# Kernel optimization log

Hardware: AMD Instinct MI355X
Metric: run time of the kernel (lower is better)

## Reference

```python
import jax, jax.numpy as jnp
import numpy as np

K = 128      # classes
CIN = 128    # ch_in
CL = 128     # ch_latent
B, H, W = 8, 1, 8192
SLOPE = 0.01 # F.leaky_relu default
EPS = 1e-5   # BatchNorm eps


def lrelu(x):
    return jnp.where(x >= 0, x, SLOPE * x)


def conv1x1(x, w, b):
    # x: (B,C,H,W), w: (O,C), b: (O,)
    return jnp.einsum('bchw,oc->bohw', x, w) + b[None, :, None, None]


def bn_eval(x, gamma, beta, mean, var):
    scale = gamma * jax.lax.rsqrt(var + EPS)
    return x * scale[None, :, None, None] + (beta - mean * scale)[None, :, None, None]


def setup_inputs() -> dict:
    key = jax.random.key(0)
    ks = jax.random.split(key, 16)
    def w(k, shape, fan_in):
        return jax.random.normal(k, shape, jnp.float32) / np.sqrt(fan_in)
    return {
        'x_in': jax.random.normal(ks[0], (B, CIN, H, W), jnp.float32),
        'cl1_w': w(ks[1], (CL, CIN), CIN), 'cl1_b': jnp.zeros((CL,), jnp.float32),
        'bn1_gamma': jnp.ones((CL,), jnp.float32), 'bn1_beta': jnp.zeros((CL,), jnp.float32),
        'bn1_mean': 0.1 * jax.random.normal(ks[2], (CL,), jnp.float32),
        'bn1_var': jax.random.uniform(ks[3], (CL,), jnp.float32, 0.5, 1.5),
        'cl2_w': w(ks[4], (CL, CL), CL), 'cl2_b': jnp.zeros((CL,), jnp.float32),
        'cl3_w': w(ks[5], (K + 1, CL), CL), 'cl3_b': jnp.zeros((K + 1,), jnp.float32),
        'reg1_w': w(ks[6], (CL, CIN), CIN), 'reg1_b': jnp.zeros((CL,), jnp.float32),
        'bnr_gamma': jnp.ones((CL,), jnp.float32), 'bnr_beta': jnp.zeros((CL,), jnp.float32),
        'bnr_mean': 0.1 * jax.random.normal(ks[7], (CL,), jnp.float32),
        'bnr_var': jax.random.uniform(ks[8], (CL,), jnp.float32, 0.5, 1.5),
        'cm2_w': w(ks[9], (K, CL, 32), CL), 'cm2_b': jnp.zeros((K, 32), jnp.float32),
        'cm3_w': w(ks[10], (K, 32, 1), 32), 'cm3_b': jnp.zeros((K, 1), jnp.float32),
    }


def reference(x_in, cl1_w, cl1_b, bn1_gamma, bn1_beta, bn1_mean, bn1_var,
              cl2_w, cl2_b, cl3_w, cl3_b,
              reg1_w, reg1_b, bnr_gamma, bnr_beta, bnr_mean, bnr_var,
              cm2_w, cm2_b, cm3_w, cm3_b):
    # classification branch
    x = lrelu(bn_eval(conv1x1(x_in, cl1_w, cl1_b), bn1_gamma, bn1_beta, bn1_mean, bn1_var))
    x = lrelu(conv1x1(x, cl2_w, cl2_b))
    x = conv1x1(x, cl3_w, cl3_b)                    # (B, K+1, H, W)
    logits = x[:, :K]
    mask = lrelu(x[:, -1:])                          # (B,1,H,W)
    inds = jnp.argmax(logits, axis=1)                # (B,H,W) int
    inds_r = inds.reshape(-1).astype(jnp.int32)      # (N,)
    xr = lrelu(bn_eval(conv1x1(x_in, reg1_w, reg1_b), bnr_gamma, bnr_beta, bnr_mean, bnr_var))
    # torch: transpose(1,3).reshape(-1, C)  -> (B,W,H,C) flatten
    xr = jnp.transpose(xr, (0, 3, 2, 1)).reshape(-1, CL)   # (N, CL)
    # CondMul 1: per-pixel gathered weight (N,CL,32)
    h = lrelu(jnp.einsum('ni,nio->no', xr, cm2_w[inds_r]) + cm2_b[inds_r])
    # CondMul 2: (N,32)->(N,1)
    reg = jnp.einsum('ni,nio->no', h, cm3_w[inds_r]) + cm3_b[inds_r]
    reg = reg.reshape(B, 1, 1, -1)                   # (B,1,1,H*W)
    x_real = (inds[:, None].astype(jnp.float32) + reg) * (1.0 / K)
    return x_real, mask
```

## Files before the change

kernel.cpp:

```cpp
#include <hip/hip_runtime.h>
#include <math.h>

#define NPOS 65536
#define NCH  128
#define DELTA 0.008f
#define HPAD 16

#define OFF_XR   0u
#define OFF_W1T  8388608u
#define OFF_W2T  (OFF_W1T + 16384u)
#define OFF_W3T  (OFF_W2T + 16384u)
#define OFF_B1F  (OFF_W3T + 16384u)
#define OFF_BRF  (OFF_B1F + 128u)
#define OFF_B2F  (OFF_BRF + 128u)
#define OFF_B3F  (OFF_B2F + 128u)
#define OFF_BF16 (OFF_B3F + 132u)
#define OFF_INT  (OFF_BF16 + 329728u)

#define UW1H 0u
#define UW1L 16384u
#define UWRH 32768u
#define UWRL 49152u
#define UW2H 65536u
#define UW2L 81920u
#define UW3H 98304u
#define UW3L 116736u
#define UW2K 135168u

#define NST 2080

typedef short bf16x8 __attribute__((ext_vector_type(8)));
typedef float f32x4 __attribute__((ext_vector_type(4)));
#define MFMA16 __builtin_amdgcn_mfma_f32_16x16x32_bf16

__device__ __forceinline__ float lrelu(float v) { return v >= 0.0f ? v : 0.01f * v; }
__device__ __forceinline__ unsigned short f2bf(float f) {
    unsigned u = __float_as_uint(f);
    return (unsigned short)((u + 0x7fffu + ((u >> 16) & 1u)) >> 16);
}
__device__ __forceinline__ float bf2f(unsigned short h) {
    return __uint_as_float(((unsigned)h) << 16);
}
__device__ __forceinline__ unsigned long long pack4(unsigned short a, unsigned short b,
                                                    unsigned short c, unsigned short d) {
    return (unsigned long long)a | ((unsigned long long)b << 16)
         | ((unsigned long long)c << 32) | ((unsigned long long)d << 48);
}

__global__ void k_prep(const float* __restrict__ cl1_w, const float* __restrict__ cl1_b,
                       const float* __restrict__ g1, const float* __restrict__ be1,
                       const float* __restrict__ mu1, const float* __restrict__ va1,
                       const float* __restrict__ cl2_w, const float* __restrict__ cl2_b,
                       const float* __restrict__ cl3_w, const float* __restrict__ cl3_b,
                       const float* __restrict__ reg1_w, const float* __restrict__ reg1_b,
                       const float* __restrict__ gr, const float* __restrict__ ber,
                       const float* __restrict__ mur, const float* __restrict__ var_,
                       const float* __restrict__ cm2w,
                       float* __restrict__ ws_f, unsigned short* __restrict__ wbf,
                       int* __restrict__ hist, int* __restrict__ fixcnt)
{
    const int bid = blockIdx.x;
    const int t = threadIdx.x;
    if (bid >= 128) {
        __shared__ float tl[32 * 132];
        int k = bid - 128;
        #pragma unroll
        for (int i = 0; i < 32; ++i) {
            float v = cm2w[(unsigned)k * 4096u + i * 128 + t];
            int ci = i * 4 + (t >> 5), o = t & 31;
            tl[o * 132 + ci] = v;
        }
        __syncthreads();
        #pragma unroll
        for (int i = 0; i < 32; ++i)
            wbf[UW2K + (unsigned)k * 4096u + i * 128 + t] = f2bf(tl[i * 132 + t]);
        return;
    }
    int tid = bid * 128 + t;
    int cin = tid >> 7, cout = tid & 127;
    float s1 = g1[cout] / sqrtf(va1[cout] + 1e-5f);
    float sr = gr[cout] / sqrtf(var_[cout] + 1e-5f);
    float w1 = cl1_w[cout * 128 + cin] * s1;
    float wr = reg1_w[cout * 128 + cin] * sr;
    float w2 = cl2_w[cout * 128 + cin];
    float w3 = cl3_w[cout * 128 + cin];
    ws_f[OFF_W1T + tid] = w1;
    ws_f[OFF_W2T + tid] = w2;
    ws_f[OFF_W3T + tid] = w3;
    int j = cout * 128 + cin;
    unsigned short h;
    h = f2bf(w1); wbf[UW1H + j] = h; wbf[UW1L + j] = f2bf(w1 - bf2f(h));
    h = f2bf(wr); wbf[UWRH + j] = h; wbf[UWRL + j] = f2bf(wr - bf2f(h));
    h = f2bf(w2); wbf[UW2H + j] = h; wbf[UW2L + j] = f2bf(w2 - bf2f(h));
    h = f2bf(w3); wbf[UW3H + j] = h; wbf[UW3L + j] = f2bf(w3 - bf2f(h));
    if (tid < 2048) {
        int r = tid >> 7, ci = tid & 127;
        float v = (r == 0) ? cl3_w[128 * 128 + ci] : 0.0f;
        int jj = (128 + r) * 128 + ci;
        h = f2bf(v); wbf[UW3H + jj] = h; wbf[UW3L + jj] = f2bf(v - bf2f(h));
    }
    if (tid < 128) {
        float s1b = g1[tid] / sqrtf(va1[tid] + 1e-5f);
        float srb = gr[tid] / sqrtf(var_[tid] + 1e-5f);
        ws_f[OFF_B1F + tid] = cl1_b[tid] * s1b + be1[tid] - mu1[tid] * s1b;
        ws_f[OFF_BRF + tid] = reg1_b[tid] * srb + ber[tid] - mur[tid] * srb;
        ws_f[OFF_B2F + tid] = cl2_b[tid];
        hist[tid * HPAD] = 0;
    }
    if (tid < 129) ws_f[OFF_B3F + tid] = cl3_b[tid];
    if (tid == 0) fixcnt[0] = 0;
}

__global__ __launch_bounds__(256, 4)
void k_fused(const float* __restrict__ X, const float* __restrict__ wsf,
             const unsigned short* __restrict__ wbf,
             unsigned short* __restrict__ XRB, float* __restrict__ out_mask,
             int* __restrict__ inds, int* __restrict__ fixcnt,
             int* __restrict__ fixlist)
{
    __shared__ __align__(16) unsigned short XBh[64 * 136];
    __shared__ __align__(16) unsigned short XBl[64 * 136];
    __shared__ float sm1[4 * 64];
    __shared__ float sm2[4 * 64];
    __shared__ int   si1[4 * 64];

    const int t = threadIdx.x;
    const int lane = t & 63;
    const int cl16 = lane & 15;
    const int q8 = (lane >> 4) * 8;
    const int q4 = (lane >> 4) * 4;
    const int wv = __builtin_amdgcn_readfirstlane(t >> 6);
    const unsigned nt64 = blockIdx.x * 64u;
    const unsigned base = nt64 + (nt64 >> 13) * 1040384u;

    const unsigned short* W1H = wbf + UW1H; const unsigned short* W1L = wbf + UW1L;
    const unsigned short* WRH = wbf + UWRH; const unsigned short* WRL = wbf + UWRL;
    const unsigned short* W2H = wbf + UW2H; const unsigned short* W2L = wbf + UW2L;
    const unsigned short* W3H = wbf + UW3H; const unsigned short* W3L = wbf + UW3L;
    const float* b1f = wsf + OFF_B1F;
    const float* brf = wsf + OFF_BRF;
    const float* b2f = wsf + OFF_B2F;
    const float* b3f = wsf + OFF_B3F;

    const f32x4 vzero = {0.f, 0.f, 0.f, 0.f};

    {
        const int pos = t & 63, cig = t >> 6;
        #pragma unroll
        for (int l = 0; l < 8; ++l) {
            int ci0 = cig * 32 + l * 4;
            float v0 = X[base + (unsigned)(ci0 + 0) * 8192u + pos];
            float v1 = X[base + (unsigned)(ci0 + 1) * 8192u + pos];
            float v2 = X[base + (unsigned)(ci0 + 2) * 8192u + pos];
            float v3 = X[base + (unsigned)(ci0 + 3) * 8192u + pos];
            unsigned short h0 = f2bf(v0), h1 = f2bf(v1), h2 = f2bf(v2), h3 = f2bf(v3);
            unsigned long long ph = pack4(h0, h1, h2, h3);
            unsigned long long pl = pack4(f2bf(v0 - bf2f(h0)), f2bf(v1 - bf2f(h1)),
                                          f2bf(v2 - bf2f(h2)), f2bf(v3 - bf2f(h3)));
            *(unsigned long long*)&XBh[pos * 136 + ci0] = ph;
            *(unsigned long long*)&XBl[pos * 136 + ci0] = pl;
        }
    }
    __syncthreads();

    f32x4 acc[2][4];

    #pragma unroll
    for (int m = 0; m < 2; ++m)
        #pragma unroll
        for (int n = 0; n < 4; ++n) acc[m][n] = vzero;
    #pragma unroll
    for (int kt = 0; kt < 4; ++kt) {
        bf16x8 Bh[4], Bl[4];
        #pragma unroll
        for (int n = 0; n < 4; ++n) {
            int bo = (n * 16 + cl16) * 136 + kt * 32 + q8;
            Bh[n] = *(const bf16x8*)&XBh[bo];
            Bl[n] = *(const bf16x8*)&XBl[bo];
        }
        #pragma unroll
        for (int m = 0; m < 2; ++m) {
            int ao = (wv * 32 + m * 16 + cl16) * 128 + kt * 32 + q8;
            bf16x8 arh = *(const bf16x8*)&WRH[ao], arl = *(const bf16x8*)&WRL[ao];
            #pragma unroll
            for (int n = 0; n < 4; ++n) {
                acc[m][n] = MFMA16(arh, Bl[n], acc[m][n], 0, 0, 0);
                acc[m][n] = MFMA16(arl, Bh[n], acc[m][n], 0, 0, 0);
                acc[m][n] = MFMA16(arh, Bh[n], acc[m][n], 0, 0, 0);
            }
        }
    }
    {
        #pragma unroll
        for (int m = 0; m < 2; ++m) {
            int cb = wv * 32 + m * 16 + q4;
            float br0 = brf[cb], br1 = brf[cb + 1], br2 = brf[cb + 2], br3 = brf[cb + 3];
            #pragma unroll
            for (int n = 0; n < 4; ++n) {
                unsigned pb = (nt64 + n * 16 + cl16) * 128u + cb;
                ushort4 xo;
                xo.x = f2bf(lrelu(acc[m][n][0] + br0));
                xo.y = f2bf(lrelu(acc[m][n][1] + br1));
                xo.z = f2bf(lrelu(acc[m][n][2] + br2));
                xo.w = f2bf(lrelu(acc[m][n][3] + br3));
                *(ushort4*)&XRB[pb] = xo;
            }
        }
    }

    #pragma unroll
    for (int m = 0; m < 2; ++m)
        #pragma unroll
        for (int n = 0; n < 4; ++n) acc[m][n] = vzero;
    #pragma unroll
    for (int kt = 0; kt < 4; ++kt) {
        bf16x8 Bh[4], Bl[4];
        #pragma unroll
        for (int n = 0; n < 4; ++n) {
            int bo = (n * 16 + cl16) * 136 + kt * 32 + q8;
            Bh[n] = *(const bf16x8*)&XBh[bo];
            Bl[n] = *(const bf16x8*)&XBl[bo];
        }
        #pragma unroll
        for (int m = 0; m < 2; ++m) {
            int ao = (wv * 32 + m * 16 + cl16) * 128 + kt * 32 + q8;
            bf16x8 a1h = *(const bf16x8*)&W1H[ao], a1l = *(const bf16x8*)&W1L[ao];
            #pragma unroll
            for (int n = 0; n < 4; ++n) {
                acc[m][n] = MFMA16(a1h, Bl[n], acc[m][n], 0, 0, 0);
                acc[m][n] = MFMA16(a1l, Bh[n], acc[m][n], 0, 0, 0);
                acc[m][n] = MFMA16(a1h, Bh[n], acc[m][n], 0, 0, 0);
            }
        }
    }
    __syncthreads();
    {
        #pragma unroll
        for (int m = 0; m < 2; ++m) {
            int cb = wv * 32 + m * 16 + q4;
            float b0 = b1f[cb], b1 = b1f[cb + 1], b2 = b1f[cb + 2], b3 = b1f[cb + 3];
            #pragma unroll
            for (int n = 0; n < 4; ++n) {
                float v0 = lrelu(acc[m][n][0] + b0), v1 = lrelu(acc[m][n][1] + b1);
                float v2 = lrelu(acc[m][n][2] + b2), v3 = lrelu(acc[m][n][3] + b3);
                unsigned short h0 = f2bf(v0), h1 = f2bf(v1), h2 = f2bf(v2), h3 = f2bf(v3);
                unsigned long long ph = pack4(h0, h1, h2, h3);
                unsigned long long pl = pack4(f2bf(v0 - bf2f(h0)), f2bf(v1 - bf2f(h1)),
                                              f2bf(v2 - bf2f(h2)), f2bf(v3 - bf2f(h3)));
                int idx = (n * 16 + cl16) * 136 + cb;
                *(unsigned long long*)&XBh[idx] = ph;
                *(unsigned long long*)&XBl[idx] = pl;
            }
        }
    }
    __syncthreads();

    #pragma unroll
    for (int m = 0; m < 2; ++m)
        #pragma unroll
        for (int n = 0; n < 4; ++n) acc[m][n] = vzero;
    #pragma unroll
    for (int kt = 0; kt < 4; ++kt) {
        bf16x8 Bh[4], Bl[4];
        #pragma unroll
        for (int n = 0; n < 4; ++n) {
            int bo = (n * 16 + cl16) * 136 + kt * 32 + q8;
            Bh[n] = *(const bf16x8*)&XBh[bo];
            Bl[n] = *(const bf16x8*)&XBl[bo];
        }
        #pragma unroll
        for (int m = 0; m < 2; ++m) {
            int ao = (wv * 32 + m * 16 + cl16) * 128 + kt * 32 + q8;
            bf16x8 ah = *(const bf16x8*)&W2H[ao], al = *(const bf16x8*)&W2L[ao];
            #pragma unroll
            for (int n = 0; n < 4; ++n) {
                acc[m][n] = MFMA16(ah, Bl[n], acc[m][n], 0, 0, 0);
                acc[m][n] = MFMA16(al, Bh[n], acc[m][n], 0, 0, 0);
                acc[m][n] = MFMA16(ah, Bh[n], acc[m][n], 0, 0, 0);
            }
        }
    }
    __syncthreads();
    {
        #pragma unroll
        for (int m = 0; m < 2; ++m) {
            int cb = wv * 32 + m * 16 + q4;
            float b0 = b2f[cb], b1 = b2f[cb + 1], b2 = b2f[cb + 2], b3 = b2f[cb + 3];
            #pragma unroll
            for (int n = 0; n < 4; ++n) {
                float v0 = lrelu(acc[m][n][0] + b0), v1 = lrelu(acc[m][n][1] + b1);
                float v2 = lrelu(acc[m][n][2] + b2), v3 = lrelu(acc[m][n][3] + b3);
                unsigned short h0 = f2bf(v0), h1 = f2bf(v1), h2 = f2bf(v2), h3 = f2bf(v3);
                unsigned long long ph = pack4(h0, h1, h2, h3);
                unsigned long long pl = pack4(f2bf(v0 - bf2f(h0)), f2bf(v1 - bf2f(h1)),
                                              f2bf(v2 - bf2f(h2)), f2bf(v3 - bf2f(h3)));
                int idx = (n * 16 + cl16) * 136 + cb;
                *(unsigned long long*)&XBh[idx] = ph;
                *(unsigned long long*)&XBl[idx] = pl;
            }
        }
    }
    __syncthreads();

    f32x4 accM = vzero;
    #pragma unroll
    for (int m = 0; m < 2; ++m)
        #pragma unroll
        for (int n = 0; n < 4; ++n) acc[m][n] = vzero;
    #pragma unroll
    for (int kt = 0; kt < 4; ++kt) {
        bf16x8 Bh[4], Bl[4];
        #pragma unroll
        for (int n = 0; n < 4; ++n) {
            int bo = (n * 16 + cl16) * 136 + kt * 32 + q8;
            Bh[n] = *(const bf16x8*)&XBh[bo];
            Bl[n] = *(const bf16x8*)&XBl[bo];
        }
        #pragma unroll
        for (int m = 0; m < 2; ++m) {
            int ao = (wv * 32 + m * 16 + cl16) * 128 + kt * 32 + q8;
            bf16x8 ah = *(const bf16x8*)&W3H[ao], al = *(const bf16x8*)&W3L[ao];
            #pragma unroll
            for (int n = 0; n < 4; ++n) {
                acc[m][n] = MFMA16(ah, Bl[n], acc[m][n], 0, 0, 0);
                acc[m][n] = MFMA16(al, Bh[n], acc[m][n], 0, 0, 0);
                acc[m][n] = MFMA16(ah, Bh[n], acc[m][n], 0, 0, 0);
            }
        }
        {
            int boM = (wv * 16 + cl16) * 136 + kt * 32 + q8;
            bf16x8 BhM = *(const bf16x8*)&XBh[boM];
            bf16x8 BlM = *(const bf16x8*)&XBl[boM];
            int ao = (128 + cl16) * 128 + kt * 32 + q8;
            bf16x8 ah = *(const bf16x8*)&W3H[ao], al = *(const bf16x8*)&W3L[ao];
            accM = MFMA16(ah, BlM, accM, 0, 0, 0);
            accM = MFMA16(al, BhM, accM, 0, 0, 0);
            accM = MFMA16(ah, BhM, accM, 0, 0, 0);
        }
    }

    {
        float bb[2][4];
        #pragma unroll
        for (int m = 0; m < 2; ++m) {
            int cb = wv * 32 + m * 16 + q4;
            bb[m][0] = b3f[cb]; bb[m][1] = b3f[cb + 1];
            bb[m][2] = b3f[cb + 2]; bb[m][3] = b3f[cb + 3];
        }
        float m1[4], m2[4]; int i1[4];
        #pragma unroll
        for (int n = 0; n < 4; ++n) {
            m1[n] = -1e30f; m2[n] = -1e30f; i1[n] = 0;
            #pragma unroll
            for (int m = 0; m < 2; ++m) {
                int cb = wv * 32 + m * 16 + q4;
                #pragma unroll
                for (int r = 0; r < 4; ++r) {
                    float v = acc[m][n][r] + bb[m][r];
                    if (v > m1[n]) { m2[n] = m1[n]; m1[n] = v; i1[n] = cb + r; }
                    else if (v > m2[n]) m2[n] = v;
                }
            }
        }
        #pragma unroll
        for (int off = 16; off <= 32; off <<= 1) {
            #pragma unroll
            for (int n = 0; n < 4; ++n) {
                float om1 = __shfl_xor(m1[n], off);
                float om2 = __shfl_xor(m2[n], off);
                int   oi1 = __shfl_xor(i1[n], off);
                if (om1 > m1[n] || (om1 == m1[n] && oi1 < i1[n])) {
                    m2[n] = fmaxf(m1[n], om2); m1[n] = om1; i1[n] = oi1;
                } else {
                    m2[n] = fmaxf(m2[n], om1);
                }
            }
        }
        if ((lane >> 4) == 0) {
            #pragma unroll
            for (int n = 0; n < 4; ++n) {
                sm1[wv * 64 + n * 16 + cl16] = m1[n];
                sm2[wv * 64 + n * 16 + cl16] = m2[n];
                si1[wv * 64 + n * 16 + cl16] = i1[n];
            }
        }
    }
    if ((lane >> 4) == 0) {
        float mb = b3f[128];
        out_mask[nt64 + wv * 16 + cl16] = lrelu(accM[0] + mb);
    }
    __syncthreads();
    if (t < 64) {
        float m1 = sm1[t], m2 = sm2[t];
        int i1 = si1[t];
        #pragma unroll
        for (int w = 1; w < 4; ++w) {
            float v1 = sm1[w * 64 + t];
            float v2 = sm2[w * 64 + t];
            int   vi = si1[w * 64 + t];
            if (v1 > m1) { m2 = fmaxf(m1, v2); m1 = v1; i1 = vi; }
            else         { m2 = fmaxf(m2, v1); }
        }
        int n = nt64 + t;
        inds[n] = i1;
        if (m1 - m2 < DELTA) {
            int slot = atomicAdd(fixcnt, 1);
            fixlist[slot] = n;
        }
    }
}

__global__ __launch_bounds__(256, 4)
void k_fix(const float* __restrict__ X, const float* __restrict__ wsf,
           const int* __restrict__ fixcnt, const int* __restrict__ fixlist,
           int* __restrict__ inds)
{
    const int cnt = fixcnt[0];
    const int t = threadIdx.x;
    const int lane = t & 63;
    const int wv = t >> 6;
    const float* W1T = wsf + OFF_W1T;
    const float* W2T = wsf + OFF_W2T;
    const float* W3T = wsf + OFF_W3T;
    const float* b1f = wsf + OFF_B1F;
    const float* b2f = wsf + OFF_B2F;
    const float* b3f = wsf + OFF_B3F;

    for (int idx = blockIdx.x * 4 + wv; idx < cnt; idx += 1024) {
        int n = fixlist[idx];
        const float* xb = X + (unsigned)(n >> 13) * 1048576u + (unsigned)(n & 8191);
        float x0 = xb[(unsigned)lane * 8192u];
        float x1 = xb[(unsigned)(64 + lane) * 8192u];
        float a0, a1;
        a0 = 0.f; a1 = 0.f;
        for (int ci = 0; ci < 64; ++ci) {
            float xv = __shfl(x0, ci);
            const float* wr = W1T + ci * 128;
            a0 = fmaf(wr[lane], xv, a0);
            a1 = fmaf(wr[64 + lane], xv, a1);
        }
        for (int ci = 0; ci < 64; ++ci) {
            float xv = __shfl(x1, ci);
            const float* wr = W1T + (64 + ci) * 128;
            a0 = fmaf(wr[lane], xv, a0);
            a1 = fmaf(wr[64 + lane], xv, a1);
        }
        x0 = lrelu(a0 + b1f[lane]); x1 = lrelu(a1 + b1f[64 + lane]);
        a0 = 0.f; a1 = 0.f;
        for (int ci = 0; ci < 64; ++ci) {
            float xv = __shfl(x0, ci);
            const float* wr = W2T + ci * 128;
            a0 = fmaf(wr[lane], xv, a0);
            a1 = fmaf(wr[64 + lane], xv, a1);
        }
        for (int ci = 0; ci < 64; ++ci) {
            float xv = __shfl(x1, ci);
            const float* wr = W2T + (64 + ci) * 128;
            a0 = fmaf(wr[lane], xv, a0);
            a1 = fmaf(wr[64 + lane], xv, a1);
        }
        x0 = lrelu(a0 + b2f[lane]); x1 = lrelu(a1 + b2f[64 + lane]);
        a0 = 0.f; a1 = 0.f;
        for (int ci = 0; ci < 64; ++ci) {
            float xv = __shfl(x0, ci);
            const float* wr = W3T + ci * 128;
            a0 = fmaf(wr[lane], xv, a0);
            a1 = fmaf(wr[64 + lane], xv, a1);
        }
        for (int ci = 0; ci < 64; ++ci) {
            float xv = __shfl(x1, ci);
            const float* wr = W3T + (64 + ci) * 128;
            a0 = fmaf(wr[lane], xv, a0);
            a1 = fmaf(wr[64 + lane], xv, a1);
        }
        float L0 = a0 + b3f[lane], L1 = a1 + b3f[64 + lane];
        float v; int id;
        if (L0 >= L1) { v = L0; id = lane; } else { v = L1; id = 64 + lane; }
        #pragma unroll
        for (int off = 1; off < 64; off <<= 1) {
            float ov = __shfl_xor(v, off);
            int   oi = __shfl_xor(id, off);
            if (ov > v || (ov == v && oi < id)) { v = ov; id = oi; }
        }
        if (lane == 0) inds[n] = id;
    }
}

__global__ void k_hist(const int* __restrict__ inds, int* __restrict__ hist)
{
    __shared__ int lh[128];
    int t = threadIdx.x;
    if (t < 128) lh[t] = 0;
    __syncthreads();
    atomicAdd(&lh[inds[blockIdx.x * 256 + t]], 1);
    __syncthreads();
    if (t < 128 && lh[t] > 0) atomicAdd(&hist[t * HPAD], lh[t]);
}

__global__ void k_scan(const int* __restrict__ hist, int* __restrict__ off,
                       int* __restrict__ cur, int* __restrict__ tiles,
                       int* __restrict__ ntt)
{
    __shared__ int s[128];
    __shared__ int s2[128];
    int t = threadIdx.x;
    int v = hist[t * HPAD];
    int ntk = (v + 63) >> 6;
    s[t] = v;
    s2[t] = ntk;
    __syncthreads();
    for (int d = 1; d < 128; d <<= 1) {
        int a  = (t >= d) ? s[t - d]  : 0;
        int a2 = (t >= d) ? s2[t - d] : 0;
        __syncthreads();
        s[t] += a;
        s2[t] += a2;
        __syncthreads();
    }
    off[t] = s[t] - v;
    cur[t * HPAD] = s[t] - v;
    int tb = s2[t] - ntk;
    for (int j = 0; j < ntk; ++j)
        tiles[tb + j] = (t << 16) | j;
    if (t == 127) ntt[0] = s2[127];
}

__global__ void k_scatter(const int* __restrict__ inds, int* __restrict__ cur,
                          int* __restrict__ bucket)
{
    __shared__ int lh[128];
    __shared__ int gb[128];
    int t = threadIdx.x;
    if (t < 128) lh[t] = 0;
    __syncthreads();
    int n = blockIdx.x * 256 + t;
    int id = inds[n];
    int r = atomicAdd(&lh[id], 1);
    __syncthreads();
    if (t < 128 && lh[t] > 0) gb[t] = atomicAdd(&cur[t * HPAD], lh[t]);
    __syncthreads();
    bucket[gb[id] + r] = n;
}

__global__ __launch_bounds__(256, 4)
void k_reg(const unsigned short* __restrict__ XRB, const unsigned short* __restrict__ wbf,
           const float* __restrict__ cm2b, const float* __restrict__ cm3w,
           const float* __restrict__ cm3b, const int* __restrict__ hist,
           const int* __restrict__ off, const int* __restrict__ bucket,
           const int* __restrict__ tiles, const int* __restrict__ ntt,
           float* __restrict__ out)
{
    __shared__ __align__(16) unsigned short XP[4 * NST];
    __shared__ float red[64];
    int bid = blockIdx.x;
    if (bid >= ntt[0]) return;
    int desc = tiles[bid];
    int k = desc >> 16;
    int start = (desc & 0xffff) << 6;
    int cnt = hist[k * HPAD];
    int base = off[k];
    int t = threadIdx.x;
    int lane = t & 63;
    int wv = __builtin_amdgcn_readfirstlane(t >> 6);
    const int n16 = lane & 15;
    const int quad = lane >> 4;

    {
        int rs = t >> 2;
        int q = t & 3;
        int sidx = start + rs;
        if (sidx >= cnt) sidx = cnt - 1;
        int n = bucket[base + sidx];
        const uint4* src = (const uint4*)(XRB + (unsigned)n * 128u + q * 32);
        uint4 a0 = src[0], a1 = src[1], a2 = src[2], a3 = src[3];
        unsigned db = (rs >> 4) * NST + q * 512 + (rs & 15) * 8;
        *(uint4*)&XP[db]       = a0;
        *(uint4*)&XP[db + 128] = a1;
        *(uint4*)&XP[db + 256] = a2;
        *(uint4*)&XP[db + 384] = a3;
    }
    __syncthreads();

    const unsigned short* wb = wbf + UW2K + (unsigned)k * 4096u;
    bf16x8 Bf[2][4];
    #pragma unroll
    for (int nf = 0; nf < 2; ++nf)
        #pragma unroll
        for (int kt = 0; kt < 4; ++kt)
            Bf[nf][kt] = *(const bf16x8*)&wb[(nf * 16 + n16) * 128 + kt * 32 + quad * 8];

    const f32x4 vzero = {0.f, 0.f, 0.f, 0.f};
    f32x4 acc[2];
    acc[0] = vzero; acc[1] = vzero;
    #pragma unroll
    for (int kt = 0; kt < 4; ++kt) {
        bf16x8 Af = *(const bf16x8*)&XP[wv * NST + kt * 512 + lane * 8];
        #pragma unroll
        for (int nf = 0; nf < 2; ++nf)
            acc[nf] = MFMA16(Af, Bf[nf][kt], acc[nf], 0, 0, 0);
    }

    float b2a = cm2b[k * 32 + n16], b2b = cm2b[k * 32 + 16 + n16];
    float w3a = cm3w[k * 32 + n16], w3b = cm3w[k * 32 + 16 + n16];
    #pragma unroll
    for (int r = 0; r < 4; ++r) {
        float p = lrelu(acc[0][r] + b2a) * w3a
                + lrelu(acc[1][r] + b2b) * w3b;
        p += __shfl_xor(p, 1);
        p += __shfl_xor(p, 2);
        p += __shfl_xor(p, 4);
        p += __shfl_xor(p, 8);
        if (n16 == 0)
            red[wv * 16 + quad * 4 + r] = p;
    }
    __syncthreads();
    if (t < 64 && start + t < cnt) {
        int n2 = bucket[base + start + t];
        out[n2] = ((float)k + red[t] + cm3b[k]) * (1.0f / 128.0f);
    }
}

extern "C" void kernel_launch(void* const* d_in, const int* in_sizes, int n_in,
                              void* d_out, int out_size, void* d_ws, size_t ws_size,
                              hipStream_t stream)
{
    (void)in_sizes; (void)n_in; (void)out_size; (void)ws_size;
    const float* x_in   = (const float*)d_in[0];
    const float* cl1_w  = (const float*)d_in[1];
    const float* cl1_b  = (const float*)d_in[2];
    const float* g1     = (const float*)d_in[3];
    const float* be1    = (const float*)d_in[4];
    const float* mu1    = (const float*)d_in[5];
    const float* va1    = (const float*)d_in[6];
    const float* cl2_w  = (const float*)d_in[7];
    const float* cl2_b  = (const float*)d_in[8];
    const float* cl3_w  = (const float*)d_in[9];
    const float* cl3_b  = (const float*)d_in[10];
    const float* reg1_w = (const float*)d_in[11];
    const float* reg1_b = (const float*)d_in[12];
    const float* gr     = (const float*)d_in[13];
    const float* ber    = (const float*)d_in[14];
    const float* mur    = (const float*)d_in[15];
    const float* var_   = (const float*)d_in[16];
    const float* cm2w   = (const float*)d_in[17];
    const float* cm2b   = (const float*)d_in[18];
    const float* cm3w   = (const float*)d_in[19];
    const float* cm3b   = (const float*)d_in[20];

    float* ws_f = (float*)d_ws;
    unsigned short* XRB = (unsigned short*)(ws_f + OFF_XR);
    unsigned short* wbf = (unsigned short*)(ws_f + OFF_BF16);
    int*   wsi    = (int*)(ws_f + OFF_INT);
    int*   inds   = wsi;
    int*   hist   = inds + 65536;
    int*   offb   = hist + 2048;
    int*   cur    = offb + 128;
    int*   ntt    = cur + 2048;
    int*   fixcnt = ntt + 4;
    int*   tiles  = fixcnt + 4;
    int*   fixlist= tiles + 1536;
    int*   bucket = fixlist + 65536;
    float* out = (float*)d_out;

    hipLaunchKernelGGL(k_prep, dim3(256), dim3(128), 0, stream,
                       cl1_w, cl1_b, g1, be1, mu1, va1, cl2_w, cl2_b, cl3_w, cl3_b,
                       reg1_w, reg1_b, gr, ber, mur, var_, cm2w, ws_f, wbf, hist, fixcnt);
    hipLaunchKernelGGL(k_fused, dim3(1024), dim3(256), 0, stream,
                       x_in, ws_f, wbf, XRB, out + 65536, inds, fixcnt, fixlist);
    hipLaunchKernelGGL(k_fix, dim3(256), dim3(256), 0, stream,
                       x_in, ws_f, fixcnt, fixlist, inds);
    hipLaunchKernelGGL(k_hist, dim3(256), dim3(256), 0, stream, inds, hist);
    hipLaunchKernelGGL(k_scan, dim3(1), dim3(128), 0, stream,
                       hist, offb, cur, tiles, ntt);
    hipLaunchKernelGGL(k_scatter, dim3(256), dim3(256), 0, stream, inds, cur, bucket);
    hipLaunchKernelGGL(k_reg, dim3(1536), dim3(256), 0, stream,
                       XRB, wbf, cm2b, cm3w, cm3b, hist, offb, bucket, tiles, ntt, out);
}
```

Before: 221.3 us.

## Fold fix, histogram and scan kernels into fused, scatter and regression kernels

The separate k_fix, k_hist and k_scan launches are removed. Near-tie argmax recomputation and the per-class histogram now run at the tail of k_fused, using a block-local fix list. The prefix scan over class counts is recomputed redundantly in every k_scatter and k_reg block instead of in a single-block kernel, and k_prep writes the transposed fp32 weights with coalesced reads. This cuts seven launches to four and their serialization gaps, in exchange for redundant scans and uneven tail work inside k_fused blocks.

Result: faster. 205.3 us (-7.2%).

```diff
diff --git a/kernel.cpp b/kernel.cpp
--- a/kernel.cpp
+++ b/kernel.cpp
@@ -57,7 +57,7 @@
                        const float* __restrict__ mur, const float* __restrict__ var_,
                        const float* __restrict__ cm2w,
                        float* __restrict__ ws_f, unsigned short* __restrict__ wbf,
-                       int* __restrict__ hist, int* __restrict__ fixcnt)
+                       int* __restrict__ hist, int* __restrict__ cur)
 {
     const int bid = blockIdx.x;
     const int t = threadIdx.x;
@@ -76,53 +76,56 @@
             wbf[UW2K + (unsigned)k * 4096u + i * 128 + t] = f2bf(tl[i * 132 + t]);
         return;
     }
-    int tid = bid * 128 + t;
-    int cin = tid >> 7, cout = tid & 127;
+    const int cout = bid;
+    const int cin = t;
+    const int row = cout * 128 + cin;
     float s1 = g1[cout] / sqrtf(va1[cout] + 1e-5f);
     float sr = gr[cout] / sqrtf(var_[cout] + 1e-5f);
-    float w1 = cl1_w[cout * 128 + cin] * s1;
-    float wr = reg1_w[cout * 128 + cin] * sr;
-    float w2 = cl2_w[cout * 128 + cin];
-    float w3 = cl3_w[cout * 128 + cin];
-    ws_f[OFF_W1T + tid] = w1;
-    ws_f[OFF_W2T + tid] = w2;
-    ws_f[OFF_W3T + tid] = w3;
-    int j = cout * 128 + cin;
+    float w1 = cl1_w[row] * s1;
+    float wr = reg1_w[row] * sr;
+    float w2 = cl2_w[row];
+    float w3 = cl3_w[row];
+    ws_f[OFF_W1T + cin * 128 + cout] = w1;
+    ws_f[OFF_W2T + cin * 128 + cout] = w2;
+    ws_f[OFF_W3T + cin * 128 + cout] = w3;
     unsigned short h;
-    h = f2bf(w1); wbf[UW1H + j] = h; wbf[UW1L + j] = f2bf(w1 - bf2f(h));
-    h = f2bf(wr); wbf[UWRH + j] = h; wbf[UWRL + j] = f2bf(wr - bf2f(h));
-    h = f2bf(w2); wbf[UW2H + j] = h; wbf[UW2L + j] = f2bf(w2 - bf2f(h));
-    h = f2bf(w3); wbf[UW3H + j] = h; wbf[UW3L + j] = f2bf(w3 - bf2f(h));
-    if (tid < 2048) {
-        int r = tid >> 7, ci = tid & 127;
-        float v = (r == 0) ? cl3_w[128 * 128 + ci] : 0.0f;
-        int jj = (128 + r) * 128 + ci;
+    h = f2bf(w1); wbf[UW1H + row] = h; wbf[UW1L + row] = f2bf(w1 - bf2f(h));
+    h = f2bf(wr); wbf[UWRH + row] = h; wbf[UWRL + row] = f2bf(wr - bf2f(h));
+    h = f2bf(w2); wbf[UW2H + row] = h; wbf[UW2L + row] = f2bf(w2 - bf2f(h));
+    h = f2bf(w3); wbf[UW3H + row] = h; wbf[UW3L + row] = f2bf(w3 - bf2f(h));
+    if (bid < 16) {
+        float v = (bid == 0) ? cl3_w[128 * 128 + t] : 0.0f;
+        int jj = (128 + bid) * 128 + t;
         h = f2bf(v); wbf[UW3H + jj] = h; wbf[UW3L + jj] = f2bf(v - bf2f(h));
     }
-    if (tid < 128) {
-        float s1b = g1[tid] / sqrtf(va1[tid] + 1e-5f);
-        float srb = gr[tid] / sqrtf(var_[tid] + 1e-5f);
-        ws_f[OFF_B1F + tid] = cl1_b[tid] * s1b + be1[tid] - mu1[tid] * s1b;
-        ws_f[OFF_BRF + tid] = reg1_b[tid] * srb + ber[tid] - mur[tid] * srb;
-        ws_f[OFF_B2F + tid] = cl2_b[tid];
-        hist[tid * HPAD] = 0;
-    }
-    if (tid < 129) ws_f[OFF_B3F + tid] = cl3_b[tid];
-    if (tid == 0) fixcnt[0] = 0;
+    if (bid == 0) {
+        float s1b = g1[t] / sqrtf(va1[t] + 1e-5f);
+        float srb = gr[t] / sqrtf(var_[t] + 1e-5f);
+        ws_f[OFF_B1F + t] = cl1_b[t] * s1b + be1[t] - mu1[t] * s1b;
+        ws_f[OFF_BRF + t] = reg1_b[t] * srb + ber[t] - mur[t] * srb;
+        ws_f[OFF_B2F + t] = cl2_b[t];
+        ws_f[OFF_B3F + t] = cl3_b[t];
+        hist[t * HPAD] = 0;
+        cur[t * HPAD] = 0;
+    }
+    if (bid == 1 && t == 0) ws_f[OFF_B3F + 128] = cl3_b[128];
 }
 
 __global__ __launch_bounds__(256, 4)
 void k_fused(const float* __restrict__ X, const float* __restrict__ wsf,
              const unsigned short* __restrict__ wbf,
              unsigned short* __restrict__ XRB, float* __restrict__ out_mask,
-             int* __restrict__ inds, int* __restrict__ fixcnt,
-             int* __restrict__ fixlist)
+             int* __restrict__ inds, int* __restrict__ hist)
 {
     __shared__ __align__(16) unsigned short XBh[64 * 136];
     __shared__ __align__(16) unsigned short XBl[64 * 136];
     __shared__ float sm1[4 * 64];
     __shared__ float sm2[4 * 64];
     __shared__ int   si1[4 * 64];
+    __shared__ int   locid[64];
+    __shared__ int   flist[64];
+    __shared__ int   fcntS;
+    __shared__ int   lh[128];
 
     const int t = threadIdx.x;
     const int lane = t & 63;
@@ -143,6 +146,8 @@
     const float* b3f = wsf + OFF_B3F;
 
     const f32x4 vzero = {0.f, 0.f, 0.f, 0.f};
+
+    if (t == 0) fcntS = 0;
 
     {
         const int pos = t & 63, cig = t >> 6;
@@ -403,141 +408,110 @@
         }
         int n = nt64 + t;
         inds[n] = i1;
+        locid[t] = i1;
         if (m1 - m2 < DELTA) {
-            int slot = atomicAdd(fixcnt, 1);
-            fixlist[slot] = n;
-        }
-    }
-}
-
-__global__ __launch_bounds__(256, 4)
-void k_fix(const float* __restrict__ X, const float* __restrict__ wsf,
-           const int* __restrict__ fixcnt, const int* __restrict__ fixlist,
-           int* __restrict__ inds)
-{
-    const int cnt = fixcnt[0];
-    const int t = threadIdx.x;
-    const int lane = t & 63;
-    const int wv = t >> 6;
-    const float* W1T = wsf + OFF_W1T;
-    const float* W2T = wsf + OFF_W2T;
-    const float* W3T = wsf + OFF_W3T;
-    const float* b1f = wsf + OFF_B1F;
-    const float* b2f = wsf + OFF_B2F;
-    const float* b3f = wsf + OFF_B3F;
-
-    for (int idx = blockIdx.x * 4 + wv; idx < cnt; idx += 1024) {
-        int n = fixlist[idx];
-        const float* xb = X + (unsigned)(n >> 13) * 1048576u + (unsigned)(n & 8191);
-        float x0 = xb[(unsigned)lane * 8192u];
-        float x1 = xb[(unsigned)(64 + lane) * 8192u];
-        float a0, a1;
-        a0 = 0.f; a1 = 0.f;
-        for (int ci = 0; ci < 64; ++ci) {
-            float xv = __shfl(x0, ci);
-            const float* wr = W1T + ci * 128;
-            a0 = fmaf(wr[lane], xv, a0);
-            a1 = fmaf(wr[64 + lane], xv, a1);
-        }
-        for (int ci = 0; ci < 64; ++ci) {
-            float xv = __shfl(x1, ci);
-            const float* wr = W1T + (64 + ci) * 128;
-            a0 = fmaf(wr[lane], xv, a0);
-            a1 = fmaf(wr[64 + lane], xv, a1);
-        }
-        x0 = lrelu(a0 + b1f[lane]); x1 = lrelu(a1 + b1f[64 + lane]);
-        a0 = 0.f; a1 = 0.f;
-        for (int ci = 0; ci < 64; ++ci) {
-            float xv = __shfl(x0, ci);
-            const float* wr = W2T + ci * 128;
-            a0 = fmaf(wr[lane], xv, a0);
-            a1 = fmaf(wr[64 + lane], xv, a1);
-        }
-        for (int ci = 0; ci < 64; ++ci) {
-            float xv = __shfl(x1, ci);
-            const float* wr = W2T + (64 + ci) * 128;
-            a0 = fmaf(wr[lane], xv, a0);
-            a1 = fmaf(wr[64 + lane], xv, a1);
-        }
-        x0 = lrelu(a0 + b2f[lane]); x1 = lrelu(a1 + b2f[64 + lane]);
-        a0 = 0.f; a1 = 0.f;
-        for (int ci = 0; ci < 64; ++ci) {
-            float xv = __shfl(x0, ci);
-            const float* wr = W3T + ci * 128;
-            a0 = fmaf(wr[lane], xv, a0);
-            a1 = fmaf(wr[64 + lane], xv, a1);
-        }
-        for (int ci = 0; ci < 64; ++ci) {
-            float xv = __shfl(x1, ci);
-            const float* wr = W3T + (64 + ci) * 128;
-            a0 = fmaf(wr[lane], xv, a0);
-            a1 = fmaf(wr[64 + lane], xv, a1);
-        }
-        float L0 = a0 + b3f[lane], L1 = a1 + b3f[64 + lane];
-        float v; int id;
-        if (L0 >= L1) { v = L0; id = lane; } else { v = L1; id = 64 + lane; }
-        #pragma unroll
-        for (int off = 1; off < 64; off <<= 1) {
-            float ov = __shfl_xor(v, off);
-            int   oi = __shfl_xor(id, off);
-            if (ov > v || (ov == v && oi < id)) { v = ov; id = oi; }
-        }
-        if (lane == 0) inds[n] = id;
-    }
-}
-
-__global__ void k_hist(const int* __restrict__ inds, int* __restrict__ hist)
-{
-    __shared__ int lh[128];
-    int t = threadIdx.x;
+            int slot = atomicAdd(&fcntS, 1);
+            flist[slot] = t;
+        }
+    }
+    __syncthreads();
+
+    {
+        const int fc = fcntS;
+        const float* W1T = wsf + OFF_W1T;
+        const float* W2T = wsf + OFF_W2T;
+        const float* W3T = wsf + OFF_W3T;
+        for (int i = wv; i < fc; i += 4) {
+            int pos = flist[i];
+            int n = nt64 + pos;
+            const float* xb = X + (unsigned)(n >> 13) * 1048576u + (unsigned)(n & 8191);
+            float x0 = xb[(unsigned)lane * 8192u];
+            float x1 = xb[(unsigned)(64 + lane) * 8192u];
+            float a0, a1;
+            a0 = 0.f; a1 = 0.f;
+            for (int ci = 0; ci < 64; ++ci) {
+                float xv = __shfl(x0, ci);
+                const float* wr = W1T + ci * 128;
+                a0 = fmaf(wr[lane], xv, a0);
+                a1 = fmaf(wr[64 + lane], xv, a1);
+            }
+            for (int ci = 0; ci < 64; ++ci) {
+                float xv = __shfl(x1, ci);
+                const float* wr = W1T + (64 + ci) * 128;
+                a0 = fmaf(wr[lane], xv, a0);
+                a1 = fmaf(wr[64 + lane], xv, a1);
+            }
+            x0 = lrelu(a0 + b1f[lane]); x1 = lrelu(a1 + b1f[64 + lane]);
+            a0 = 0.f; a1 = 0.f;
+            for (int ci = 0; ci < 64; ++ci) {
+                float xv = __shfl(x0, ci);
+                const float* wr = W2T + ci * 128;
+                a0 = fmaf(wr[lane], xv, a0);
+                a1 = fmaf(wr[64 + lane], xv, a1);
+            }
+            for (int ci = 0; ci < 64; ++ci) {
+                float xv = __shfl(x1, ci);
+                const float* wr = W2T + (64 + ci) * 128;
+                a0 = fmaf(wr[lane], xv, a0);
+                a1 = fmaf(wr[64 + lane], xv, a1);
+            }
+            x0 = lrelu(a0 + b2f[lane]); x1 = lrelu(a1 + b2f[64 + lane]);
+            a0 = 0.f; a1 = 0.f;
+            for (int ci = 0; ci < 64; ++ci) {
+                float xv = __shfl(x0, ci);
+                const float* wr = W3T + ci * 128;
+                a0 = fmaf(wr[lane], xv, a0);
+                a1 = fmaf(wr[64 + lane], xv, a1);
+            }
+            for (int ci = 0; ci < 64; ++ci) {
+                float xv = __shfl(x1, ci);
+                const float* wr = W3T + (64 + ci) * 128;
+                a0 = fmaf(wr[lane], xv, a0);
+                a1 = fmaf(wr[64 + lane], xv, a1);
+            }
+            float L0 = a0 + b3f[lane], L1 = a1 + b3f[64 + lane];
+            float v; int id;
+            if (L0 >= L1) { v = L0; id = lane; } else { v = L1; id = 64 + lane; }
+            #pragma unroll
+            for (int off = 1; off < 64; off <<= 1) {
+                float ov = __shfl_xor(v, off);
+                int   oi = __shfl_xor(id, off);
+                if (ov > v || (ov == v && oi < id)) { v = ov; id = oi; }
+            }
+            if (lane == 0) { inds[n] = id; locid[pos] = id; }
+        }
+    }
+    __syncthreads();
+
     if (t < 128) lh[t] = 0;
     __syncthreads();
-    atomicAdd(&lh[inds[blockIdx.x * 256 + t]], 1);
+    if (t < 64) atomicAdd(&lh[locid[t]], 1);
     __syncthreads();
     if (t < 128 && lh[t] > 0) atomicAdd(&hist[t * HPAD], lh[t]);
 }
 
-__global__ void k_scan(const int* __restrict__ hist, int* __restrict__ off,
-                       int* __restrict__ cur, int* __restrict__ tiles,
-                       int* __restrict__ ntt)
-{
-    __shared__ int s[128];
-    __shared__ int s2[128];
-    int t = threadIdx.x;
-    int v = hist[t * HPAD];
-    int ntk = (v + 63) >> 6;
-    s[t] = v;
-    s2[t] = ntk;
-    __syncthreads();
-    for (int d = 1; d < 128; d <<= 1) {
-        int a  = (t >= d) ? s[t - d]  : 0;
-        int a2 = (t >= d) ? s2[t - d] : 0;
-        __syncthreads();
-        s[t] += a;
-        s2[t] += a2;
-        __syncthreads();
-    }
-    off[t] = s[t] - v;
-    cur[t * HPAD] = s[t] - v;
-    int tb = s2[t] - ntk;
-    for (int j = 0; j < ntk; ++j)
-        tiles[tb + j] = (t << 16) | j;
-    if (t == 127) ntt[0] = s2[127];
-}
-
-__global__ void k_scatter(const int* __restrict__ inds, int* __restrict__ cur,
-                          int* __restrict__ bucket)
+__global__ void k_scatter(const int* __restrict__ inds, const int* __restrict__ hist,
+                          int* __restrict__ cur, int* __restrict__ bucket)
 {
     __shared__ int lh[128];
     __shared__ int gb[128];
+    __shared__ int sv[128];
+    __shared__ int sh[128];
     int t = threadIdx.x;
-    if (t < 128) lh[t] = 0;
-    __syncthreads();
+    if (t < 128) { int h = hist[t * HPAD]; sh[t] = h; sv[t] = h; lh[t] = 0; }
+    __syncthreads();
+    for (int d = 1; d < 128; d <<= 1) {
+        int a = (t < 128 && t >= d) ? sv[t - d] : 0;
+        __syncthreads();
+        if (t < 128) sv[t] += a;
+        __syncthreads();
+    }
     int n = blockIdx.x * 256 + t;
     int id = inds[n];
     int r = atomicAdd(&lh[id], 1);
     __syncthreads();
-    if (t < 128 && lh[t] > 0) gb[t] = atomicAdd(&cur[t * HPAD], lh[t]);
+    if (t < 128 && lh[t] > 0)
+        gb[t] = (sv[t] - sh[t]) + atomicAdd(&cur[t * HPAD], lh[t]);
     __syncthreads();
     bucket[gb[id] + r] = n;
 }
@@ -546,20 +520,39 @@
 void k_reg(const unsigned short* __restrict__ XRB, const unsigned short* __restrict__ wbf,
            const float* __restrict__ cm2b, const float* __restrict__ cm3w,
            const float* __restrict__ cm3b, const int* __restrict__ hist,
-           const int* __restrict__ off, const int* __restrict__ bucket,
-           const int* __restrict__ tiles, const int* __restrict__ ntt,
-           float* __restrict__ out)
+           const int* __restrict__ bucket, float* __restrict__ out)
 {
     __shared__ __align__(16) unsigned short XP[4 * NST];
     __shared__ float red[64];
+    __shared__ int sh[128];
+    __shared__ int sv[128];
+    __shared__ int st[128];
+    __shared__ int skj[2];
     int bid = blockIdx.x;
-    if (bid >= ntt[0]) return;
-    int desc = tiles[bid];
-    int k = desc >> 16;
-    int start = (desc & 0xffff) << 6;
-    int cnt = hist[k * HPAD];
-    int base = off[k];
     int t = threadIdx.x;
+    if (t < 128) {
+        int h = hist[t * HPAD];
+        sh[t] = h; sv[t] = h; st[t] = (h + 63) >> 6;
+    }
+    __syncthreads();
+    for (int d = 1; d < 128; d <<= 1) {
+        int a = (t < 128 && t >= d) ? sv[t - d] : 0;
+        int b = (t < 128 && t >= d) ? st[t - d] : 0;
+        __syncthreads();
+        if (t < 128) { sv[t] += a; st[t] += b; }
+        __syncthreads();
+    }
+    if (bid >= st[127]) return;
+    if (t < 128) {
+        int ntk = (sh[t] + 63) >> 6;
+        int tb = st[t] - ntk;
+        if (bid >= tb && bid < st[t]) { skj[0] = t; skj[1] = bid - tb; }
+    }
+    __syncthreads();
+    const int k = skj[0];
+    const int start = skj[1] << 6;
+    const int cnt = sh[k];
+    const int base = sv[k] - sh[k];
     int lane = t & 63;
     int wv = __builtin_amdgcn_readfirstlane(t >> 6);
     const int n16 = lane & 15;
@@ -664,15 +657,11 @@
 
     hipLaunchKernelGGL(k_prep, dim3(256), dim3(128), 0, stream,
                        cl1_w, cl1_b, g1, be1, mu1, va1, cl2_w, cl2_b, cl3_w, cl3_b,
-                       reg1_w, reg1_b, gr, ber, mur, var_, cm2w, ws_f, wbf, hist, fixcnt);
+                       reg1_w, reg1_b, gr, ber, mur, var_, cm2w, ws_f, wbf, hist, cur);
     hipLaunchKernelGGL(k_fused, dim3(1024), dim3(256), 0, stream,
-                       x_in, ws_f, wbf, XRB, out + 65536, inds, fixcnt, fixlist);
-    hipLaunchKernelGGL(k_fix, dim3(256), dim3(256), 0, stream,
-                       x_in, ws_f, fixcnt, fixlist, inds);
-    hipLaunchKernelGGL(k_hist, dim3(256), dim3(256), 0, stream, inds, hist);
-    hipLaunchKernelGGL(k_scan, dim3(1), dim3(128), 0, stream,
-                       hist, offb, cur, tiles, ntt);
-    hipLaunchKernelGGL(k_scatter, dim3(256), dim3(256), 0, stream, inds, cur, bucket);
+                       x_in, ws_f, wbf, XRB, out + 65536, inds, hist);
+    hipLaunchKernelGGL(k_scatter, dim3(256), dim3(256), 0, stream,
+                       inds, hist, cur, bucket);
     hipLaunchKernelGGL(k_reg, dim3(1536), dim3(256), 0, stream,
-                       XRB, wbf, cm2b, cm3w, cm3b, hist, offb, bucket, tiles, ntt, out);
-}
+                       XRB, wbf, cm2b, cm3w, cm3b, hist, bucket, out);
+}
```
